# Performance work log

Measured on AMD Instinct MI355X. Metric: run time of the kernel, lower is better.

The kernel has to match this reference:

```python
import jax, jax.numpy as jnp
import numpy as np

D_MODEL, D_HEAD, N_HEAD = 1024, 64, 16
B, T1, T2 = 2, 2048, 2048


def setup_inputs() -> dict:
    key = jax.random.key(0)
    ks = jax.random.split(key, 8)
    s = 1.0 / np.sqrt(D_MODEL)
    return {
        "x": jax.random.normal(ks[0], (B, T1, D_MODEL), dtype=jnp.float32),
        "context": jax.random.normal(ks[1], (B, T2, D_MODEL), dtype=jnp.float32),
        "bias": jax.random.normal(ks[2], (T1, T2), dtype=jnp.float32),
        "W_q": jax.random.normal(ks[3], (D_MODEL, N_HEAD * D_HEAD), dtype=jnp.float32) * s,
        "W_k": jax.random.normal(ks[4], (D_MODEL, N_HEAD * D_HEAD), dtype=jnp.float32) * s,
        "W_v": jax.random.normal(ks[5], (D_MODEL, N_HEAD * D_HEAD), dtype=jnp.float32) * s,
        "W_out": jax.random.normal(ks[6], (N_HEAD * D_HEAD, D_MODEL), dtype=jnp.float32) * s,
        "b_out": jnp.zeros((D_MODEL,), dtype=jnp.float32),
    }


def reference(x, context, bias, W_q, W_k, W_v, W_out, b_out):
    Bq, T1_, _ = x.shape
    T2_ = context.shape[1]
    atten_scale = 1.0 / np.sqrt(D_HEAD)
    # fixed (non-trainable) per-head scale: 2^{-1}, ..., 2^{-n_head}
    head_scale = jnp.exp2(-jnp.arange(1, N_HEAD + 1, dtype=jnp.float32))

    # projections -> [B, H, T, d]
    q = (x @ W_q).reshape(Bq, T1_, N_HEAD, D_HEAD).transpose(0, 2, 1, 3)
    k = (context @ W_k).reshape(Bq, T2_, N_HEAD, D_HEAD).transpose(0, 2, 1, 3)
    v = (context @ W_v).reshape(Bq, T2_, N_HEAD, D_HEAD).transpose(0, 2, 1, 3)

    # scores: [B, H, T1, T2]
    scores = jnp.einsum("bhqd,bhkd->bhqk", q, k) * atten_scale
    scores = scores + bias[None, None, :, :] * head_scale[None, :, None, None]
    attn = jax.nn.softmax(scores, axis=-1)

    out = jnp.einsum("bhqk,bhkd->bqhd", attn, v).reshape(Bq, T1_, N_HEAD * D_HEAD)
    # dropout is identity in eval mode
    return out @ W_out + b_out
```

## Files before the change

kernel.cpp:

```cpp
#include <hip/hip_runtime.h>

typedef float  f32x4   __attribute__((ext_vector_type(4)));
typedef float  f32x16  __attribute__((ext_vector_type(16)));
typedef __bf16 bf16x8  __attribute__((ext_vector_type(8)));
typedef __bf16 bf16x2  __attribute__((ext_vector_type(2)));
typedef short  short8v __attribute__((ext_vector_type(8)));
typedef unsigned uint4v __attribute__((ext_vector_type(4)));

__device__ __forceinline__ short f2bf(float f) {
  unsigned u = __float_as_uint(f);
  unsigned r = (u + 0x7FFFu + ((u >> 16) & 1u)) >> 16;
  return (short)r;
}

__device__ __forceinline__ f32x4 mfma16(bf16x8 a, bf16x8 b, f32x4 c) {
  return __builtin_amdgcn_mfma_f32_16x16x32_bf16(a, b, c, 0, 0, 0);
}
__device__ __forceinline__ f32x16 mfma32(bf16x8 a, bf16x8 b, f32x16 c) {
  return __builtin_amdgcn_mfma_f32_32x32x16_bf16(a, b, c, 0, 0, 0);
}

__device__ __forceinline__ void gload16(const void* g, void* l) {
  __builtin_amdgcn_global_load_lds(
      (const __attribute__((address_space(1))) unsigned int*)g,
      (__attribute__((address_space(3))) unsigned int*)l,
      16, 0, 0);
}

__device__ __forceinline__ bf16x8 p_exchange(const unsigned* pk, int a, int hi) {
  unsigned y1 = hi ? pk[4 * a + 0] : pk[4 * a + 2];
  unsigned z1 = __shfl_xor(y1, 32);
  unsigned y2 = hi ? pk[4 * a + 1] : pk[4 * a + 3];
  unsigned z2 = __shfl_xor(y2, 32);
  unsigned w0 = hi ? z1 : pk[4 * a + 0];
  unsigned w1 = hi ? z2 : pk[4 * a + 1];
  unsigned w2 = hi ? pk[4 * a + 2] : z1;
  unsigned w3 = hi ? pk[4 * a + 3] : z2;
  uint4v q4 = {w0, w1, w2, w3};
  return __builtin_bit_cast(bf16x8, q4);
}


__global__ __launch_bounds__(256) void cvt_copy(const float* __restrict__ in,
                                                short* __restrict__ out, int n4) {
  int i = blockIdx.x * blockDim.x + threadIdx.x;
  int stride = gridDim.x * blockDim.x;
  for (; i < n4; i += stride) {
    float4 v = *(const float4*)&in[i * 4];
    short4 o;
    o.x = f2bf(v.x); o.y = f2bf(v.y); o.z = f2bf(v.z); o.w = f2bf(v.w);
    *(short4*)&out[i * 4] = o;
  }
}

__global__ __launch_bounds__(256) void cvt_transpose4(const float* __restrict__ W0,
                                                      const float* __restrict__ W1,
                                                      const float* __restrict__ W2,
                                                      const float* __restrict__ W3,
                                                      short* __restrict__ T0,
                                                      short* __restrict__ T1,
                                                      short* __restrict__ T2,
                                                      short* __restrict__ T3) {
  __shared__ short t_s[64][72];
  int z = blockIdx.z;
  const float* W = (z == 0) ? W0 : (z == 1) ? W1 : (z == 2) ? W2 : W3;
  short* Wt = (z == 0) ? T0 : (z == 1) ? T1 : (z == 2) ? T2 : T3;
  int k0 = blockIdx.y * 64, n0 = blockIdx.x * 64;
  int tid = threadIdx.x;
#pragma unroll
  for (int i = 0; i < 4; i++) {
    int idx = i * 256 + tid;
    int r = idx >> 4, cg = idx & 15;
    float4 v = *(const float4*)&W[(k0 + r) * 1024 + n0 + cg * 4];
    t_s[cg * 4 + 0][r] = f2bf(v.x);
    t_s[cg * 4 + 1][r] = f2bf(v.y);
    t_s[cg * 4 + 2][r] = f2bf(v.z);
    t_s[cg * 4 + 3][r] = f2bf(v.w);
  }
  __syncthreads();
#pragma unroll
  for (int i = 0; i < 2; i++) {
    int idx = i * 256 + tid;
    int r = idx >> 3, cg = idx & 7;
    short8v val = *(short8v*)&t_s[r][cg * 8];
    *(short8v*)&Wt[(n0 + r) * 1024 + k0 + cg * 8] = val;
  }
}

template <int EPI>
__global__ __launch_bounds__(256, 4) void gemm_bf16(const short* __restrict__ A,
                                                    const short* __restrict__ Bt,
                                                    void* __restrict__ out,
                                                    void* __restrict__ out2,
                                                    const float* __restrict__ bout) {
  constexpr int KD = 1024;
  constexpr int NB = (EPI == 3) ? 32 : 16;
  __shared__ short a_s[64][64];
  __shared__ short b_s[64][64];
  int tid = threadIdx.x, w = tid >> 6, lane = tid & 63;
  int g = lane >> 4, c16 = lane & 15;
  int hsw = c16 & 7;

  int lin = blockIdx.x + NB * blockIdx.y;
  int wk = (lin & 7) * (NB * 8) + (lin >> 3);
  int c0 = (wk & (NB - 1)) * 64, r0 = (wk / NB) * 64;

  int wr = (w >> 1) * 32, wc = (w & 1) * 32;
  f32x4 acc[2][2] = {};

  for (int kt = 0; kt < KD / 64; ++kt) {
    int k0 = kt * 64;
    __syncthreads();
#pragma unroll
    for (int i = 0; i < 2; i++) {
      int cb = i * 256 + w * 64;
      int c = cb + lane;
      int row = c >> 3, kg = c & 7;
      int sw = (kg ^ (row & 7)) * 8;
      gload16(A + (r0 + row) * KD + k0 + sw, (char*)a_s + cb * 16);
      gload16(Bt + (c0 + row) * KD + k0 + sw, (char*)b_s + cb * 16);
    }
    __syncthreads();
#pragma unroll
    for (int kk = 0; kk < 2; kk++) {
      bf16x8 af[2], bf[2];
      int sl0 = ((4 * kk + g) ^ hsw) * 8;
#pragma unroll
      for (int m = 0; m < 2; m++) af[m] = *(const bf16x8*)&a_s[wr + m * 16 + c16][sl0];
#pragma unroll
      for (int n = 0; n < 2; n++) bf[n] = *(const bf16x8*)&b_s[wc + n * 16 + c16][sl0];
#pragma unroll
      for (int m = 0; m < 2; m++)
#pragma unroll
        for (int n = 0; n < 2; n++) acc[m][n] = mfma16(af[m], bf[n], acc[m][n]);
    }
  }

#pragma unroll
  for (int m = 0; m < 2; m++)
#pragma unroll
    for (int n = 0; n < 2; n++)
#pragma unroll
      for (int r = 0; r < 4; r++) {
        int row = r0 + wr + m * 16 + g * 4 + r;
        int col = c0 + wc + n * 16 + c16;
        float v = acc[m][n][r];
        int b = row >> 11, t = row & 2047;
        if (EPI == 2) {
          ((float*)out)[row * 1024 + col] = v + bout[col];
        } else if (EPI == 0) {
          int h = col >> 6, d = col & 63;
          ((short*)out)[(((b * 16 + h) * 2048) + t) * 64 + d] = f2bf(v);
        } else {
          if (col < 1024) {
            int h = col >> 6, d = col & 63;
            ((short*)out)[(((b * 16 + h) * 2048) + t) * 64 + d] = f2bf(v);
          } else {
            int cv = col - 1024;
            int h = cv >> 6, d = cv & 63;
            ((short*)out2)[(((b * 16 + h) * 64) + d) * 2048 + t] = f2bf(v);
          }
        }
      }
}

__global__ __launch_bounds__(256, 4) void flash_attn(const short* __restrict__ Qg,
                                                     const short* __restrict__ Kg,
                                                     const short* __restrict__ Vtg,
                                                     const float* __restrict__ bias,
                                                     short* __restrict__ Og) {
  __shared__ short k_s[2][64][64];
  __shared__ short v_s[2][64][64];

  int tid = threadIdx.x, w = tid >> 6, lane = tid & 63;
  int hi = lane >> 5, ll = lane & 31;
  int l7 = ll & 7;

  int lin = blockIdx.x + 16 * (blockIdx.y + 16 * blockIdx.z);
  int wk = (lin & 7) * 64 + (lin >> 3);
  int qb = (wk & 15) * 128;
  int h = (wk >> 4) & 15;
  int b = wk >> 8;

  const short* Qh = Qg + (size_t)(b * 16 + h) * 2048 * 64;
  const short* Kh = Kg + (size_t)(b * 16 + h) * 2048 * 64;
  const short* Vh = Vtg + (size_t)(b * 16 + h) * 64 * 2048;

  const float C1 = 0.125f * 1.44269504f;
  const float C2 = exp2f(-(float)(h + 1)) * 1.44269504f;

  int qrow = qb + w * 32 + ll;
  const float* bp = bias + (size_t)qrow * 2048 + 4 * hi;

#pragma unroll
  for (int i = 0; i < 2; i++) {
    int cb = i * 256 + w * 64;
    int c = cb + lane;
    int row = c >> 3, t8 = c & 7, sw = (t8 ^ (row & 7)) * 8;
    gload16(Kh + row * 64 + sw, (char*)&k_s[0][0][0] + cb * 16);
    gload16(Vh + row * 2048 + sw, (char*)&v_s[0][0][0] + cb * 16);
  }
  bf16x8 qf[4];
#pragma unroll
  for (int dm = 0; dm < 4; dm++)
    qf[dm] = *(const bf16x8*)(Qh + (size_t)qrow * 64 + dm * 16 + hi * 8);
  asm volatile("" ::: "memory");

  float l_run = 0.f;
  f32x16 o_acc[2] = {};

  for (int kt = 0; kt < 32; ++kt) {
    int cur = kt & 1;
    f32x4 bv0[4];
#pragma unroll
    for (int u = 0; u < 4; u++)
      bv0[u] = *(const f32x4*)(bp + kt * 64 + u * 8);

    if (kt < 31) {
      const short* Ks = Kh + (size_t)(kt + 1) * 64 * 64;
      const short* Vs = Vh + (kt + 1) * 64;
#pragma unroll
      for (int i = 0; i < 2; i++) {
        int cb = i * 256 + w * 64;
        int c = cb + lane;
        int row = c >> 3, t8 = c & 7, sw = (t8 ^ (row & 7)) * 8;
        gload16(Ks + row * 64 + sw, (char*)&k_s[cur ^ 1][0][0] + cb * 16);
        gload16(Vs + row * 2048 + sw, (char*)&v_s[cur ^ 1][0][0] + cb * 16);
      }
    }
    asm volatile("s_waitcnt vmcnt(8)" ::: "memory");
    __builtin_amdgcn_s_barrier();

    f32x16 sacc = {};
    __builtin_amdgcn_s_setprio(1);
#pragma unroll
    for (int dm = 0; dm < 4; dm++) {
      const short* kr = &k_s[cur][ll][((2 * dm + hi) ^ l7) * 8];
      sacc = mfma32(*(const bf16x8*)kr, qf[dm], sacc);
    }
    __builtin_amdgcn_s_setprio(0);

    float lp = 0.f;
    unsigned pk[8];
#pragma unroll
    for (int i = 0; i < 8; i++) {
      float p0 = exp2f(sacc[2 * i] * C1 + bv0[i >> 1][2 * (i & 1)] * C2);
      float p1 = exp2f(sacc[2 * i + 1] * C1 + bv0[i >> 1][2 * (i & 1) + 1] * C2);
      lp += p0 + p1;
      bf16x2 pp = {(__bf16)p0, (__bf16)p1};
      pk[i] = __builtin_bit_cast(unsigned, pp);
    }
    l_run += lp;

    f32x4 bv1[4];
#pragma unroll
    for (int u = 0; u < 4; u++)
      bv1[u] = *(const f32x4*)(bp + kt * 64 + 32 + u * 8);

    __builtin_amdgcn_s_setprio(1);
#pragma unroll
    for (int a = 0; a < 2; a++) {
      bf16x8 PA = p_exchange(pk, a, hi);
#pragma unroll
      for (int dt = 0; dt < 2; dt++) {
        const short* vr = &v_s[cur][dt * 32 + ll][((2 * a + hi) ^ l7) * 8];
        o_acc[dt] = mfma32(PA, *(const bf16x8*)vr, o_acc[dt]);
      }
    }
    __builtin_amdgcn_s_setprio(0);
    asm volatile("" ::: "memory");

    f32x16 sacc1 = {};
    __builtin_amdgcn_s_setprio(1);
#pragma unroll
    for (int dm = 0; dm < 4; dm++) {
      const short* kr = &k_s[cur][32 + ll][((2 * dm + hi) ^ l7) * 8];
      sacc1 = mfma32(*(const bf16x8*)kr, qf[dm], sacc1);
    }
    __builtin_amdgcn_s_setprio(0);

    float lp1 = 0.f;
#pragma unroll
    for (int i = 0; i < 8; i++) {
      float p0 = exp2f(sacc1[2 * i] * C1 + bv1[i >> 1][2 * (i & 1)] * C2);
      float p1 = exp2f(sacc1[2 * i + 1] * C1 + bv1[i >> 1][2 * (i & 1) + 1] * C2);
      lp1 += p0 + p1;
      bf16x2 pp = {(__bf16)p0, (__bf16)p1};
      pk[i] = __builtin_bit_cast(unsigned, pp);
    }
    l_run += lp1;

    __builtin_amdgcn_s_setprio(1);
#pragma unroll
    for (int a = 0; a < 2; a++) {
      bf16x8 PA = p_exchange(pk, a, hi);
#pragma unroll
      for (int dt = 0; dt < 2; dt++) {
        const short* vr = &v_s[cur][dt * 32 + ll][((4 + 2 * a + hi) ^ l7) * 8];
        o_acc[dt] = mfma32(PA, *(const bf16x8*)vr, o_acc[dt]);
      }
    }
    __builtin_amdgcn_s_setprio(0);
    __builtin_amdgcn_s_barrier();
  }

  l_run += __shfl_xor(l_run, 32);
  float invl = 1.f / l_run;

#pragma unroll
  for (int r = 0; r < 16; r++) {
    int q = (r & 3) + 8 * (r >> 2) + 4 * hi;
    float iv = __shfl(invl, q);
    int tg = qb + w * 32 + q;
#pragma unroll
    for (int dt = 0; dt < 2; dt++) {
      Og[(size_t)(b * 2048 + tg) * 1024 + h * 64 + dt * 32 + ll] =
          f2bf(o_acc[dt][r] * iv);
    }
  }
}

extern "C" void kernel_launch(void* const* d_in, const int* in_sizes, int n_in,
                              void* d_out, int out_size, void* d_ws, size_t ws_size,
                              hipStream_t stream) {
  const float* x    = (const float*)d_in[0];
  const float* ctx  = (const float*)d_in[1];
  const float* bias = (const float*)d_in[2];
  const float* Wq   = (const float*)d_in[3];
  const float* Wk   = (const float*)d_in[4];
  const float* Wv   = (const float*)d_in[5];
  const float* Wo   = (const float*)d_in[6];
  const float* bo   = (const float*)d_in[7];
  float* out = (float*)d_out;

  char* ws = (char*)d_ws;
  short* x_bf = (short*)(ws + 0);
  short* c_bf = (short*)(ws + 8388608);
  short* wq_t = (short*)(ws + 16777216);
  short* wk_t = (short*)(ws + 18874368);
  short* wv_t = (short*)(ws + 20971520);
  short* wo_t = (short*)(ws + 23068672);
  short* q_ws = (short*)(ws + 25165824);
  short* k_ws = (short*)(ws + 33554432);
  short* v_ws = (short*)(ws + 41943040);
  short* o_ws = (short*)(ws + 50331648);

  cvt_copy<<<1024, 256, 0, stream>>>(x, x_bf, 1048576);
  cvt_copy<<<1024, 256, 0, stream>>>(ctx, c_bf, 1048576);
  dim3 tg(16, 16, 4);
  cvt_transpose4<<<tg, 256, 0, stream>>>(Wq, Wk, Wv, Wo, wq_t, wk_t, wv_t, wo_t);

  dim3 gq(16, 64);
  gemm_bf16<0><<<gq, 256, 0, stream>>>(x_bf, wq_t, q_ws, nullptr, nullptr);
  dim3 gkv(32, 64);
  gemm_bf16<3><<<gkv, 256, 0, stream>>>(c_bf, wk_t, k_ws, v_ws, nullptr);

  dim3 fg(16, 16, 2);
  flash_attn<<<fg, 256, 0, stream>>>(q_ws, k_ws, v_ws, bias, o_ws);

  gemm_bf16<2><<<gq, 256, 0, stream>>>(o_ws, wo_t, out, nullptr, bo);
}
```

Measured before the change: 180.1 us.

## Convert attention bias to bf16 and remap blocks for bias reuse

```diff
diff --git a/kernel.cpp b/kernel.cpp
--- a/kernel.cpp
+++ b/kernel.cpp
@@ -3,6 +3,7 @@
 typedef float  f32x4   __attribute__((ext_vector_type(4)));
 typedef float  f32x16  __attribute__((ext_vector_type(16)));
 typedef __bf16 bf16x8  __attribute__((ext_vector_type(8)));
+typedef __bf16 bf16x4  __attribute__((ext_vector_type(4)));
 typedef __bf16 bf16x2  __attribute__((ext_vector_type(2)));
 typedef short  short8v __attribute__((ext_vector_type(8)));
 typedef unsigned uint4v __attribute__((ext_vector_type(4)));
@@ -167,7 +168,7 @@
 __global__ __launch_bounds__(256, 4) void flash_attn(const short* __restrict__ Qg,
                                                      const short* __restrict__ Kg,
                                                      const short* __restrict__ Vtg,
-                                                     const float* __restrict__ bias,
+                                                     const short* __restrict__ biasb,
                                                      short* __restrict__ Og) {
   __shared__ short k_s[2][64][64];
   __shared__ short v_s[2][64][64];
@@ -177,10 +178,10 @@
   int l7 = ll & 7;
 
   int lin = blockIdx.x + 16 * (blockIdx.y + 16 * blockIdx.z);
-  int wk = (lin & 7) * 64 + (lin >> 3);
-  int qb = (wk & 15) * 128;
-  int h = (wk >> 4) & 15;
-  int b = wk >> 8;
+  int qi = (lin & 7) | (((lin >> 8) & 1) << 3);
+  int h = (lin >> 3) & 15;
+  int b = (lin >> 7) & 1;
+  int qb = qi * 128;
 
   const short* Qh = Qg + (size_t)(b * 16 + h) * 2048 * 64;
   const short* Kh = Kg + (size_t)(b * 16 + h) * 2048 * 64;
@@ -190,7 +191,7 @@
   const float C2 = exp2f(-(float)(h + 1)) * 1.44269504f;
 
   int qrow = qb + w * 32 + ll;
-  const float* bp = bias + (size_t)qrow * 2048 + 4 * hi;
+  const short* bp = biasb + (size_t)qrow * 2048 + 4 * hi;
 
 #pragma unroll
   for (int i = 0; i < 2; i++) {
@@ -211,10 +212,10 @@
 
   for (int kt = 0; kt < 32; ++kt) {
     int cur = kt & 1;
-    f32x4 bv0[4];
+    bf16x4 bv0[4];
 #pragma unroll
     for (int u = 0; u < 4; u++)
-      bv0[u] = *(const f32x4*)(bp + kt * 64 + u * 8);
+      bv0[u] = *(const bf16x4*)(bp + kt * 64 + u * 8);
 
     if (kt < 31) {
       const short* Ks = Kh + (size_t)(kt + 1) * 64 * 64;
@@ -244,18 +245,20 @@
     unsigned pk[8];
 #pragma unroll
     for (int i = 0; i < 8; i++) {
-      float p0 = exp2f(sacc[2 * i] * C1 + bv0[i >> 1][2 * (i & 1)] * C2);
-      float p1 = exp2f(sacc[2 * i + 1] * C1 + bv0[i >> 1][2 * (i & 1) + 1] * C2);
+      float b0 = (float)bv0[i >> 1][2 * (i & 1)];
+      float b1 = (float)bv0[i >> 1][2 * (i & 1) + 1];
+      float p0 = exp2f(sacc[2 * i] * C1 + b0 * C2);
+      float p1 = exp2f(sacc[2 * i + 1] * C1 + b1 * C2);
       lp += p0 + p1;
       bf16x2 pp = {(__bf16)p0, (__bf16)p1};
       pk[i] = __builtin_bit_cast(unsigned, pp);
     }
     l_run += lp;
 
-    f32x4 bv1[4];
+    bf16x4 bv1[4];
 #pragma unroll
     for (int u = 0; u < 4; u++)
-      bv1[u] = *(const f32x4*)(bp + kt * 64 + 32 + u * 8);
+      bv1[u] = *(const bf16x4*)(bp + kt * 64 + 32 + u * 8);
 
     __builtin_amdgcn_s_setprio(1);
 #pragma unroll
@@ -282,8 +285,10 @@
     float lp1 = 0.f;
 #pragma unroll
     for (int i = 0; i < 8; i++) {
-      float p0 = exp2f(sacc1[2 * i] * C1 + bv1[i >> 1][2 * (i & 1)] * C2);
-      float p1 = exp2f(sacc1[2 * i + 1] * C1 + bv1[i >> 1][2 * (i & 1) + 1] * C2);
+      float b0 = (float)bv1[i >> 1][2 * (i & 1)];
+      float b1 = (float)bv1[i >> 1][2 * (i & 1) + 1];
+      float p0 = exp2f(sacc1[2 * i] * C1 + b0 * C2);
+      float p1 = exp2f(sacc1[2 * i + 1] * C1 + b1 * C2);
       lp1 += p0 + p1;
       bf16x2 pp = {(__bf16)p0, (__bf16)p1};
       pk[i] = __builtin_bit_cast(unsigned, pp);
@@ -344,6 +349,7 @@
   short* k_ws = (short*)(ws + 33554432);
   short* v_ws = (short*)(ws + 41943040);
   short* o_ws = (short*)(ws + 50331648);
+  short* bias_bf = x_bf;
 
   cvt_copy<<<1024, 256, 0, stream>>>(x, x_bf, 1048576);
   cvt_copy<<<1024, 256, 0, stream>>>(ctx, c_bf, 1048576);
@@ -355,8 +361,10 @@
   dim3 gkv(32, 64);
   gemm_bf16<3><<<gkv, 256, 0, stream>>>(c_bf, wk_t, k_ws, v_ws, nullptr);
 
+  cvt_copy<<<1024, 256, 0, stream>>>(bias, bias_bf, 1048576);
+
   dim3 fg(16, 16, 2);
-  flash_attn<<<fg, 256, 0, stream>>>(q_ws, k_ws, v_ws, bias, o_ws);
+  flash_attn<<<fg, 256, 0, stream>>>(q_ws, k_ws, v_ws, bias_bf, o_ws);
 
   gemm_bf16<2><<<gq, 256, 0, stream>>>(o_ws, wo_t, out, nullptr, bo);
 }
```

After: 188.2 us. +4.5%, slower.
